# Kernel tuning notes

Hardware: AMD Instinct MI355X
Metric: run time of the kernel (lower is better)

Reference implementation:

```python
import jax, jax.numpy as jnp
import numpy as np

N_NODES = 16384   # dim_size (number of aggregation groups)
DEG = 16          # neighbors per node
H = 128           # hidden_dim
E = N_NODES * DEG # total neighbor rows


def setup_inputs() -> dict:
    key = jax.random.key(0)
    k1, k2, k3 = jax.random.split(key, 3)
    x = jax.random.normal(k1, (E, H), dtype=jnp.float32)
    # sorted segment ids, DEG neighbors per node (ragged in general; uniform here)
    index = jnp.repeat(jnp.arange(N_NODES, dtype=jnp.int32), DEG)
    # torch LSTM params: gates stacked [i, f, g, o] -> [4H, H]
    W_ih = jax.random.normal(k2, (4 * H, H), dtype=jnp.float32) * 0.02  # xavier gain=0.02 scale
    W_hh = jax.random.normal(k3, (4 * H, H), dtype=jnp.float32) * (1.0 / np.sqrt(H))
    b_ih = jnp.zeros((4 * H,), jnp.float32)
    b_hh = jnp.zeros((4 * H,), jnp.float32)
    return {"x": x, "index": index, "W_ih": W_ih, "W_hh": W_hh,
            "b_ih": b_ih, "b_hh": b_hh, "dim_size": N_NODES}


def reference(x, index, W_ih, W_hh, b_ih, b_hh, dim_size):
    # Faithful to LSTMAggregator.forward: per-group gather of neighbor rows,
    # single-layer LSTM over each group's sequence, final hidden state h_n
    # written to out[group]; empty groups stay zero. (The original's randperm
    # shuffle is nondeterministic and omitted: neighbors kept in index order.)
    x = jnp.nan_to_num(x, nan=0.0)
    E_, Hd = x.shape

    # --- pack ragged groups into a padded [N, L, H] tensor ---
    order = jnp.argsort(index, stable=True)
    idx_s = index[order]
    counts = jax.ops.segment_sum(jnp.ones((E_,), jnp.int32), idx_s, num_segments=dim_size)
    starts = jnp.cumsum(counts) - counts           # exclusive prefix sum
    pos = jnp.arange(E_, dtype=jnp.int32) - starts[idx_s]  # position within group
    L = int(jnp.max(counts))                       # static at call time (concrete inputs)

    x_s = x[order]
    padded = jnp.zeros((dim_size, L, Hd), x.dtype).at[idx_s, pos].set(x_s)  # [N, L, H]
    valid = jnp.arange(L)[None, :] < counts[:, None]                        # [N, L]

    # --- batched masked LSTM scan over time ---
    bias = b_ih + b_hh
    h0 = jnp.zeros((dim_size, Hd), x.dtype)

    def step(carry, inp):
        h, c = carry
        xt, m = inp                                 # xt: [N, H], m: [N]
        gates = xt @ W_ih.T + h @ W_hh.T + bias     # [N, 4H], gate order i,f,g,o
        i, f, g, o = jnp.split(gates, 4, axis=-1)
        i = jax.nn.sigmoid(i); f = jax.nn.sigmoid(f)
        g = jnp.tanh(g);       o = jax.nn.sigmoid(o)
        c_new = f * c + i * g
        h_new = o * jnp.tanh(c_new)
        m = m[:, None]
        return (jnp.where(m, h_new, h), jnp.where(m, c_new, c)), None

    xs = (jnp.swapaxes(padded, 0, 1), valid.T)      # time-major [L, N, H], [L, N]
    (h_final, _), _ = jax.lax.scan(step, (h0, h0), xs)
    return jnp.nan_to_num(h_final, nan=0.0)        # [dim_size, H]
```

## Files before the change

### kernel.cpp

```cpp
#include <hip/hip_runtime.h>

#define DEG      16
#define HDIM     128
#define MB       64
#define NTHREADS 512

typedef __attribute__((ext_vector_type(8))) short  short8;
typedef __attribute__((ext_vector_type(4))) float  floatx4;

__device__ __forceinline__ unsigned short f2bf(float f) {
  union { float f; unsigned int u; } v; v.f = f;
  unsigned int u = v.u;
  u += 0x7fffu + ((u >> 16) & 1u);
  return (unsigned short)(u >> 16);
}

__device__ __forceinline__ float fsig(float x) {
  return __builtin_amdgcn_rcpf(1.0f + __expf(-x));
}
__device__ __forceinline__ float ftanh(float x) {
  return 1.0f - 2.0f * __builtin_amdgcn_rcpf(1.0f + __expf(2.0f * x));
}

__global__ void convert_w_kernel(const float* __restrict__ Wih,
                                 const float* __restrict__ Whh,
                                 unsigned short* __restrict__ Wsw) {
  int i    = blockIdx.x * 256 + threadIdx.x;
  int lane = i & 63;
  int frag = i >> 6;
  int kt = frag >> 5;
  int wg = frag & 31;
  int w  = wg >> 2;
  int g  = wg & 3;
  int j  = g * 128 + w * 16 + (lane & 15);
  int k0 = kt * 32 + (lane >> 4) * 8;
  const float* src = (k0 < HDIM) ? (Wih + (size_t)j * HDIM + k0)
                                 : (Whh + (size_t)j * HDIM + (k0 - HDIM));
  short8 o;
  #pragma unroll
  for (int e = 0; e < 8; ++e) o[e] = (short)f2bf(src[e]);
  *(short8*)(Wsw + (size_t)i * 8) = o;
}

__global__ __launch_bounds__(NTHREADS, 2)
void lstm_agg_kernel(const float* __restrict__ x,
                     const float* __restrict__ b_ih,
                     const float* __restrict__ b_hh,
                     const unsigned short* __restrict__ Wsw,
                     float* __restrict__ out) {
  __shared__ __align__(16) unsigned short As[MB * 256];

  const int tid  = threadIdx.x;
  const int w_id = tid >> 6;
  const int lane = tid & 63;
  const int l15  = lane & 15;
  const int q    = lane >> 4;
  const int node0 = blockIdx.x * MB;

  const int j_g = w_id * 16 + l15;

  float bias[4];
  #pragma unroll
  for (int g = 0; g < 4; ++g) bias[g] = b_ih[g * 128 + j_g] + b_hh[g * 128 + j_g];

  short8 breg[3][4];
  #pragma unroll
  for (int kt = 0; kt < 3; ++kt)
    #pragma unroll
    for (int g = 0; g < 4; ++g) {
      int fi = kt * 32 + w_id * 4 + g;
      breg[kt][g] = *(const short8*)(Wsw + ((size_t)fi * 64 + lane) * 8);
    }

  floatx4 c[4], h[4];
  #pragma unroll
  for (int mt = 0; mt < 4; ++mt) {
    floatx4 z = {0.0f, 0.0f, 0.0f, 0.0f};
    c[mt] = z; h[mt] = z;
  }

  const int m_x = tid >> 3;
  const int kc  = tid & 7;
  const float* xbase = x + ((size_t)(node0 + m_x) * DEG) * HDIM + kc * 16;

  floatx4 xp[4];
  #pragma unroll
  for (int v = 0; v < 4; ++v) xp[v] = ((const floatx4*)xbase)[v];

  #pragma unroll 1
  for (int t = 0; t < DEG; ++t) {
    {
      short8 p0, p1;
      #pragma unroll
      for (int e = 0; e < 4; ++e) {
        p0[e]     = (short)f2bf(xp[0][e]);
        p0[e + 4] = (short)f2bf(xp[1][e]);
        p1[e]     = (short)f2bf(xp[2][e]);
        p1[e + 4] = (short)f2bf(xp[3][e]);
      }
      int ms = m_x & 7;
      int c0 = (kc * 2) ^ ms;
      int c1 = (kc * 2 + 1) ^ ms;
      *(short8*)&As[m_x * 256 + c0 * 8] = p0;
      *(short8*)&As[m_x * 256 + c1 * 8] = p1;
    }
    {
      const int kk = HDIM + j_g;
      const int chunk = kk >> 3;
      const int kl = kk & 7;
      #pragma unroll
      for (int mt = 0; mt < 4; ++mt)
        #pragma unroll
        for (int r = 0; r < 4; ++r) {
          int m = mt * 16 + q * 4 + r;
          As[m * 256 + ((chunk ^ (m & 7)) << 3) + kl] = f2bf(h[mt][r]);
        }
    }
    __syncthreads();

    if (t + 1 < DEG) {
      const float* xb = xbase + (size_t)(t + 1) * HDIM;
      #pragma unroll
      for (int v = 0; v < 4; ++v) xp[v] = ((const floatx4*)xb)[v];
    }

    const unsigned short* Wp = Wsw;
    asm volatile("" : "+s"(Wp));

    floatx4 acc[4][4];
    #pragma unroll
    for (int g = 0; g < 4; ++g) {
      floatx4 bv = {bias[g], bias[g], bias[g], bias[g]};
      #pragma unroll
      for (int mt = 0; mt < 4; ++mt) acc[g][mt] = bv;
    }

    #pragma unroll
    for (int kt = 0; kt < 8; ++kt) {
      short8 af[4];
      #pragma unroll
      for (int mt = 0; mt < 4; ++mt) {
        int m = mt * 16 + l15;
        int chunk = (kt * 4 + q) ^ (m & 7);
        af[mt] = *(const short8*)&As[m * 256 + chunk * 8];
      }
      short8 bfr[4];
      if (kt < 3) {
        #pragma unroll
        for (int g = 0; g < 4; ++g) bfr[g] = breg[kt][g];
      } else {
        #pragma unroll
        for (int g = 0; g < 4; ++g) {
          int fi = kt * 32 + w_id * 4 + g;
          bfr[g] = *(const short8*)(Wp + ((size_t)fi * 64 + lane) * 8);
        }
      }
      #pragma unroll
      for (int g = 0; g < 4; ++g)
        #pragma unroll
        for (int mt = 0; mt < 4; ++mt)
          acc[g][mt] = __builtin_amdgcn_mfma_f32_16x16x32_bf16(af[mt], bfr[g], acc[g][mt], 0, 0, 0);
    }
    __syncthreads();

    #pragma unroll
    for (int mt = 0; mt < 4; ++mt)
      #pragma unroll
      for (int r = 0; r < 4; ++r) {
        float iv = fsig (acc[0][mt][r]);
        float fv = fsig (acc[1][mt][r]);
        float gv = ftanh(acc[2][mt][r]);
        float ov = fsig (acc[3][mt][r]);
        float cn = fv * c[mt][r] + iv * gv;
        c[mt][r] = cn;
        h[mt][r] = ov * ftanh(cn);
      }
  }

  #pragma unroll
  for (int mt = 0; mt < 4; ++mt)
    #pragma unroll
    for (int r = 0; r < 4; ++r) {
      int m = mt * 16 + q * 4 + r;
      out[(size_t)(node0 + m) * HDIM + j_g] = h[mt][r];
    }
}

extern "C" void kernel_launch(void* const* d_in, const int* in_sizes, int n_in,
                              void* d_out, int out_size, void* d_ws, size_t ws_size,
                              hipStream_t stream) {
  const float* x   = (const float*)d_in[0];
  const float* Wih = (const float*)d_in[2];
  const float* Whh = (const float*)d_in[3];
  const float* bih = (const float*)d_in[4];
  const float* bhh = (const float*)d_in[5];
  unsigned short* Wsw = (unsigned short*)d_ws;
  float* out = (float*)d_out;

  hipLaunchKernelGGL(convert_w_kernel, dim3(64), dim3(256), 0, stream, Wih, Whh, Wsw);

  int nodes   = in_sizes[0] / (DEG * HDIM);
  int nblocks = nodes / MB;
  hipLaunchKernelGGL(lstm_agg_kernel, dim3(nblocks), dim3(NTHREADS), 0, stream,
                     x, bih, bhh, Wsw, out);
}
```

Measured before the change: 288.2 us.

## Halve node tile, double-buffer LDS, drop second barrier per timestep

Cuts the node tile per block from 64 to 32 and raises the launch-bounds occupancy target from 2 to 4 blocks per CU. The shared A tile (x_t and h) is now double-buffered, so the next step's inputs are written to the alternate buffer after the gate math, which removes one __syncthreads per timestep. The x row for step t+2 is prefetched into registers one step earlier than before. More blocks are launched and every block still loads the full weight fragments, which adds L2 traffic, while the tighter register budget could cause spills.

```diff
diff --git a/kernel.cpp b/kernel.cpp
--- a/kernel.cpp
+++ b/kernel.cpp
@@ -2,7 +2,7 @@
 
 #define DEG      16
 #define HDIM     128
-#define MB       64
+#define MB       32
 #define NTHREADS 512
 
 typedef __attribute__((ext_vector_type(8))) short  short8;
@@ -42,13 +42,13 @@
   *(short8*)(Wsw + (size_t)i * 8) = o;
 }
 
-__global__ __launch_bounds__(NTHREADS, 2)
+__global__ __launch_bounds__(NTHREADS, 4)
 void lstm_agg_kernel(const float* __restrict__ x,
                      const float* __restrict__ b_ih,
                      const float* __restrict__ b_hh,
                      const unsigned short* __restrict__ Wsw,
                      float* __restrict__ out) {
-  __shared__ __align__(16) unsigned short As[MB * 256];
+  __shared__ __align__(16) unsigned short As[2][MB * 256];
 
   const int tid  = threadIdx.x;
   const int w_id = tid >> 6;
@@ -72,77 +72,64 @@
       breg[kt][g] = *(const short8*)(Wsw + ((size_t)fi * 64 + lane) * 8);
     }
 
-  floatx4 c[4], h[4];
-  #pragma unroll
-  for (int mt = 0; mt < 4; ++mt) {
+  floatx4 c[2], h[2];
+  #pragma unroll
+  for (int mt = 0; mt < 2; ++mt) {
     floatx4 z = {0.0f, 0.0f, 0.0f, 0.0f};
     c[mt] = z; h[mt] = z;
   }
 
-  const int m_x = tid >> 3;
-  const int kc  = tid & 7;
-  const float* xbase = x + ((size_t)(node0 + m_x) * DEG) * HDIM + kc * 16;
-
-  floatx4 xp[4];
-  #pragma unroll
-  for (int v = 0; v < 4; ++v) xp[v] = ((const floatx4*)xbase)[v];
+  const int m_x = tid >> 4;
+  const int kc  = tid & 15;
+  const float* xbase = x + ((size_t)(node0 + m_x) * DEG) * HDIM + kc * 8;
+  const int xch = (kc ^ (m_x & 7)) * 8;
+  const int hchunk = (HDIM + j_g) >> 3;
+  const int hkl = j_g & 7;
+
+  floatx4 xp0 = ((const floatx4*)xbase)[0];
+  floatx4 xp1 = ((const floatx4*)xbase)[1];
+
+  {
+    short8 p;
+    #pragma unroll
+    for (int e = 0; e < 4; ++e) { p[e] = (short)f2bf(xp0[e]); p[e + 4] = (short)f2bf(xp1[e]); }
+    *(short8*)&As[0][m_x * 256 + xch] = p;
+    unsigned short hz = f2bf(0.0f);
+    #pragma unroll
+    for (int mt = 0; mt < 2; ++mt)
+      #pragma unroll
+      for (int r = 0; r < 4; ++r) {
+        int m = mt * 16 + q * 4 + r;
+        As[0][m * 256 + ((hchunk ^ (m & 7)) << 3) + hkl] = hz;
+      }
+  }
+  xp0 = ((const floatx4*)(xbase + HDIM))[0];
+  xp1 = ((const floatx4*)(xbase + HDIM))[1];
 
   #pragma unroll 1
   for (int t = 0; t < DEG; ++t) {
-    {
-      short8 p0, p1;
-      #pragma unroll
-      for (int e = 0; e < 4; ++e) {
-        p0[e]     = (short)f2bf(xp[0][e]);
-        p0[e + 4] = (short)f2bf(xp[1][e]);
-        p1[e]     = (short)f2bf(xp[2][e]);
-        p1[e + 4] = (short)f2bf(xp[3][e]);
-      }
-      int ms = m_x & 7;
-      int c0 = (kc * 2) ^ ms;
-      int c1 = (kc * 2 + 1) ^ ms;
-      *(short8*)&As[m_x * 256 + c0 * 8] = p0;
-      *(short8*)&As[m_x * 256 + c1 * 8] = p1;
-    }
-    {
-      const int kk = HDIM + j_g;
-      const int chunk = kk >> 3;
-      const int kl = kk & 7;
-      #pragma unroll
-      for (int mt = 0; mt < 4; ++mt)
-        #pragma unroll
-        for (int r = 0; r < 4; ++r) {
-          int m = mt * 16 + q * 4 + r;
-          As[m * 256 + ((chunk ^ (m & 7)) << 3) + kl] = f2bf(h[mt][r]);
-        }
-    }
     __syncthreads();
-
-    if (t + 1 < DEG) {
-      const float* xb = xbase + (size_t)(t + 1) * HDIM;
-      #pragma unroll
-      for (int v = 0; v < 4; ++v) xp[v] = ((const floatx4*)xb)[v];
-    }
+    const int buf = t & 1;
 
     const unsigned short* Wp = Wsw;
     asm volatile("" : "+s"(Wp));
 
-    floatx4 acc[4][4];
+    floatx4 acc[4][2];
     #pragma unroll
     for (int g = 0; g < 4; ++g) {
       floatx4 bv = {bias[g], bias[g], bias[g], bias[g]};
       #pragma unroll
-      for (int mt = 0; mt < 4; ++mt) acc[g][mt] = bv;
+      for (int mt = 0; mt < 2; ++mt) acc[g][mt] = bv;
     }
 
     #pragma unroll
     for (int kt = 0; kt < 8; ++kt) {
-      short8 af[4];
-      #pragma unroll
-      for (int mt = 0; mt < 4; ++mt) {
+      short8 af[2];
+      #pragma unroll
+      for (int mt = 0; mt < 2; ++mt) {
         int m = mt * 16 + l15;
         int chunk = (kt * 4 + q) ^ (m & 7);
-        af[mt] = *(const short8*)&As[m * 256 + chunk * 8];
+        af[mt] = *(const short8*)&As[buf][m * 256 + chunk * 8];
       }
       short8 bfr[4];
       if (kt < 3) {
@@ -158,13 +145,12 @@
       #pragma unroll
       for (int g = 0; g < 4; ++g)
         #pragma unroll
-        for (int mt = 0; mt < 4; ++mt)
+        for (int mt = 0; mt < 2; ++mt)
           acc[g][mt] = __builtin_amdgcn_mfma_f32_16x16x32_bf16(af[mt], bfr[g], acc[g][mt], 0, 0, 0);
     }
-    __syncthreads();
-
-    #pragma unroll
-    for (int mt = 0; mt < 4; ++mt)
+
+    #pragma unroll
+    for (int mt = 0; mt < 2; ++mt)
       #pragma unroll
       for (int r = 0; r < 4; ++r) {
         float iv = fsig (acc[0][mt][r]);
@@ -175,10 +161,29 @@
         c[mt][r] = cn;
         h[mt][r] = ov * ftanh(cn);
       }
+
+    if (t + 1 < DEG) {
+      short8 p;
+      #pragma unroll
+      for (int e = 0; e < 4; ++e) { p[e] = (short)f2bf(xp0[e]); p[e + 4] = (short)f2bf(xp1[e]); }
+      *(short8*)&As[buf ^ 1][m_x * 256 + xch] = p;
+      #pragma unroll
+      for (int mt = 0; mt < 2; ++mt)
+        #pragma unroll
+        for (int r = 0; r < 4; ++r) {
+          int m = mt * 16 + q * 4 + r;
+          As[buf ^ 1][m * 256 + ((hchunk ^ (m & 7)) << 3) + hkl] = f2bf(h[mt][r]);
+        }
+      if (t + 2 < DEG) {
+        const float* xb = xbase + (size_t)(t + 2) * HDIM;
+        xp0 = ((const floatx4*)xb)[0];
+        xp1 = ((const floatx4*)xb)[1];
+      }
+    }
   }
 
   #pragma unroll
-  for (int mt = 0; mt < 4; ++mt)
+  for (int mt = 0; mt < 2; ++mt)
     #pragma unroll
     for (int r = 0; r < 4; ++r) {
       int m = mt * 16 + q * 4 + r;
```

Result: slower. 445.7 us (+54.7%).
